# Optimization experiments

Measured on AMD Instinct MI355X. Metric: run time of the kernel, lower is better.

Reference implementation:

```python
import jax, jax.numpy as jnp
import numpy as np

VOCAB = 50000
B, S = 256, 512
M1, M2, EMB = 1024, 512, 256


def setup_inputs() -> dict:
    key = jax.random.key(0)
    k_idx, k1, k2, k3, kb1, kb2, kb3 = jax.random.split(key, 7)
    idx = jax.random.randint(k_idx, (B, S), 0, VOCAB)
    # torch Linear weights are [out, in]
    W1 = jax.random.normal(k1, (M1, VOCAB), dtype=jnp.float32) * (1.0 / np.sqrt(VOCAB))
    b1 = jax.random.normal(kb1, (M1,), dtype=jnp.float32) * 0.01
    W2 = jax.random.normal(k2, (M2, M1), dtype=jnp.float32) * (1.0 / np.sqrt(M1))
    b2 = jax.random.normal(kb2, (M2,), dtype=jnp.float32) * 0.01
    W3 = jax.random.normal(k3, (EMB, M2), dtype=jnp.float32) * (1.0 / np.sqrt(M2))
    b3 = jax.random.normal(kb3, (EMB,), dtype=jnp.float32) * 0.01
    return {"idx": idx, "W1": W1, "b1": b1, "W2": W2, "b2": b2, "W3": W3, "b3": b3}


def make_bow_vector(idx, vocab_size):
    # vectorized scatter-add histogram: vec[i, idx[i, j]] += 1
    batch = idx.shape[0]
    rows = jnp.arange(batch)[:, None]  # [B, 1] broadcast against [B, S]
    return jnp.zeros((batch, vocab_size), dtype=jnp.float32).at[rows, idx].add(1.0)


def reference(idx, W1, b1, W2, b2, W3, b3):
    bow = make_bow_vector(idx, W1.shape[1])            # [B, V]
    h = jax.nn.relu(bow @ W1.T + b1)                   # [B, M1]
    h = jax.nn.relu(h @ W2.T + b2)                     # [B, M2]
    emb = jax.nn.relu(h @ W3.T + b3)                   # [B, EMB]
    return emb
```

## Files before the change

### kernel.cpp

```cpp
#include <hip/hip_runtime.h>
#include <hip/hip_bf16.h>

#define VOCAB   50000
#define BATCH   256
#define SEQ     512
#define NM1     1024
#define NM2     512
#define NEMB    256
#define KB1     782
#define KPAD    (KB1*64)
#define SPLITK  32
#define NT      16
#define HHALF   (KPAD/2)

typedef __attribute__((ext_vector_type(8))) short short8;
typedef __attribute__((ext_vector_type(4))) float f32x4;

#define BOW_BYTES   ((size_t)BATCH * KPAD * 2)
#define PART_BYTES  ((size_t)SPLITK * BATCH * NM1 * 4)

__device__ __forceinline__ short f2b(float x) {
    __hip_bfloat16 b = __float2bfloat16(x);
    return __builtin_bit_cast(short, b);
}
__device__ __forceinline__ unsigned short f2bu(float x) {
    __hip_bfloat16 b = __float2bfloat16(x);
    return __builtin_bit_cast(unsigned short, b);
}

__global__ __launch_bounds__(256) void BOW_hist2(const int* __restrict__ idx,
                                                 __hip_bfloat16* __restrict__ bow) {
    __shared__ unsigned int h[HHALF / 2];
    const int b    = blockIdx.x;
    const int row  = b >> 1;
    const int lo   = (b & 1) * HHALF;
    const int t    = threadIdx.x;

    for (int j = t; j < HHALF / 2; j += 256) h[j] = 0u;
    __syncthreads();

    #pragma unroll
    for (int u = 0; u < 2; u++) {
        int v = idx[row * SEQ + u * 256 + t];
        int d = v - lo;
        if ((unsigned)d < (unsigned)HHALF)
            atomicAdd(&h[d >> 1], (d & 1) ? 0x10000u : 1u);
    }
    __syncthreads();

    unsigned int* dst = (unsigned int*)(bow + (size_t)row * KPAD + lo);
    for (int j = t; j < HHALF / 2; j += 256) {
        unsigned int w  = h[j];
        unsigned int l16 = f2bu((float)(w & 0xFFFFu));
        unsigned int h16 = f2bu((float)(w >> 16));
        dst[j] = l16 | (h16 << 16);
    }
}

__global__ __launch_bounds__(512) void BOW_gemm1(
        const __hip_bfloat16* __restrict__ bow,
        const float* __restrict__ W1,
        float* __restrict__ partials)
{
    __shared__ __align__(16) __hip_bfloat16 As[256 * 64];
    __shared__ __align__(16) __hip_bfloat16 Bs[64 * 64];

    const int tid = threadIdx.x;
    const int bid = blockIdx.x;
    const int s   = bid >> 4;
    const int nt  = bid & 15;
    const int n0  = nt * 64;

    const int kb_start = s * 24 + (s < 14 ? s : 14);
    const int kb_count = 24 + (s < 14 ? 1 : 0);

    const int lane = tid & 63;
    const int w    = tid >> 6;
    const int wm   = w >> 1;
    const int wn   = w & 1;

    f32x4 acc[4][2];
    #pragma unroll
    for (int m = 0; m < 4; m++)
        #pragma unroll
        for (int n = 0; n < 2; n++) acc[m][n] = (f32x4){0.f, 0.f, 0.f, 0.f};

    const int brow = tid >> 3;
    const int bk8  = tid & 7;
    const int bdst = brow * 64 + ((bk8 * 8) ^ ((brow & 7) << 3));
    const float* wsrc = W1 + (size_t)(n0 + brow) * VOCAB + bk8 * 8;

    for (int kb = kb_start; kb < kb_start + kb_count; ++kb) {
        const int kg0 = kb * 64;

        #pragma unroll
        for (int i = 0; i < 4; i++) {
            int c   = i * 512 + tid;
            int row = c >> 3;
            int k8  = c & 7;
            const __hip_bfloat16* src =
                bow + (size_t)row * KPAD + kg0 + ((k8 * 8) ^ ((row & 7) << 3));
            __builtin_amdgcn_global_load_lds(
                (const __attribute__((address_space(1))) void*)src,
                (__attribute__((address_space(3))) void*)&As[c * 8], 16, 0, 0);
        }

        {
            int kg = kg0 + bk8 * 8;
            float4 v0 = {0.f,0.f,0.f,0.f}, v1 = {0.f,0.f,0.f,0.f};
            if (kg < VOCAB) {
                const float* src = wsrc + kg0;
                v0 = *reinterpret_cast<const float4*>(src);
                v1 = *reinterpret_cast<const float4*>(src + 4);
            }
            short8 p;
            p[0] = f2b(v0.x); p[1] = f2b(v0.y); p[2] = f2b(v0.z); p[3] = f2b(v0.w);
            p[4] = f2b(v1.x); p[5] = f2b(v1.y); p[6] = f2b(v1.z); p[7] = f2b(v1.w);
            *reinterpret_cast<short8*>(&Bs[bdst]) = p;
        }
        __syncthreads();

        #pragma unroll
        for (int kk = 0; kk < 2; kk++) {
            short8 a[4], b[2];
            const int kf = kk * 32 + ((lane >> 4) << 3);
            #pragma unroll
            for (int m = 0; m < 4; m++) {
                int row = wm * 64 + m * 16 + (lane & 15);
                int e   = row * 64 + (kf ^ ((row & 7) << 3));
                a[m] = *reinterpret_cast<const short8*>(&As[e]);
            }
            #pragma unroll
            for (int n = 0; n < 2; n++) {
                int row = wn * 32 + n * 16 + (lane & 15);
                int e   = row * 64 + (kf ^ ((row & 7) << 3));
                b[n] = *reinterpret_cast<const short8*>(&Bs[e]);
            }
            #pragma unroll
            for (int m = 0; m < 4; m++)
                #pragma unroll
                for (int n = 0; n < 2; n++)
                    acc[m][n] = __builtin_amdgcn_mfma_f32_16x16x32_bf16(
                                    a[m], b[n], acc[m][n], 0, 0, 0);
        }
        __syncthreads();
    }

    float* dst = partials + (size_t)s * (BATCH * NM1);
    #pragma unroll
    for (int m = 0; m < 4; m++) {
        #pragma unroll
        for (int n = 0; n < 2; n++) {
            int col = n0 + wn * 32 + n * 16 + (lane & 15);
            #pragma unroll
            for (int j = 0; j < 4; j++) {
                int rowi = wm * 64 + m * 16 + ((lane >> 4) * 4 + j);
                dst[(size_t)rowi * NM1 + col] = acc[m][n][j];
            }
        }
    }
}

__global__ void BOW_reduce1(const float* __restrict__ partials,
                            const float* __restrict__ b1,
                            float* __restrict__ h1) {
    int o = blockIdx.x * 256 + threadIdx.x;
    int m = o & (NM1 - 1);
    float s = b1[m];
    #pragma unroll
    for (int sp = 0; sp < SPLITK; sp++) s += partials[(size_t)sp * (BATCH * NM1) + o];
    h1[o] = fmaxf(s, 0.f);
}

__global__ void BOW_gemm_f32(const float* __restrict__ A,
                             const float* __restrict__ Bw,
                             const float* __restrict__ bias,
                             float* __restrict__ out,
                             int N, int K) {
    __shared__ float As[32][33];
    __shared__ float Bs[32][33];
    int tid = threadIdx.x;
    int i0 = blockIdx.y * 32, n0 = blockIdx.x * 32;
    int r = tid >> 5, c = tid & 31;
    int ty = tid >> 4, tx = tid & 15;
    float a2[2][2] = {{0.f, 0.f}, {0.f, 0.f}};

    for (int k0 = 0; k0 < K; k0 += 32) {
        #pragma unroll
        for (int rr = 0; rr < 4; rr++) {
            As[r + rr * 8][c] = A[(size_t)(i0 + r + rr * 8) * K + k0 + c];
            Bs[r + rr * 8][c] = Bw[(size_t)(n0 + r + rr * 8) * K + k0 + c];
        }
        __syncthreads();
        #pragma unroll
        for (int k = 0; k < 32; k++) {
            float av0 = As[ty * 2][k],     av1 = As[ty * 2 + 1][k];
            float bv0 = Bs[tx * 2][k],     bv1 = Bs[tx * 2 + 1][k];
            a2[0][0] += av0 * bv0; a2[0][1] += av0 * bv1;
            a2[1][0] += av1 * bv0; a2[1][1] += av1 * bv1;
        }
        __syncthreads();
    }
    #pragma unroll
    for (int ii = 0; ii < 2; ii++)
        #pragma unroll
        for (int nn = 0; nn < 2; nn++) {
            int i = i0 + ty * 2 + ii, n = n0 + tx * 2 + nn;
            out[(size_t)i * N + n] = fmaxf(a2[ii][nn] + bias[n], 0.f);
        }
}

extern "C" void kernel_launch(void* const* d_in, const int* in_sizes, int n_in,
                              void* d_out, int out_size, void* d_ws, size_t ws_size,
                              hipStream_t stream) {
    const int*   idx = (const int*)d_in[0];
    const float* W1  = (const float*)d_in[1];
    const float* b1  = (const float*)d_in[2];
    const float* W2  = (const float*)d_in[3];
    const float* b2  = (const float*)d_in[4];
    const float* W3  = (const float*)d_in[5];
    const float* b3  = (const float*)d_in[6];
    float* out = (float*)d_out;

    char* ws = (char*)d_ws;
    __hip_bfloat16* bow = (__hip_bfloat16*)ws;
    float* partials = (float*)(ws + BOW_BYTES);
    float* h1       = (float*)(ws + BOW_BYTES + PART_BYTES);
    float* h2       = h1 + BATCH * NM1;

    BOW_hist2<<<BATCH * 2, 256, 0, stream>>>(idx, bow);
    BOW_gemm1<<<SPLITK * NT, 512, 0, stream>>>(bow, W1, partials);
    BOW_reduce1<<<(BATCH * NM1) / 256, 256, 0, stream>>>(partials, b1, h1);
    BOW_gemm_f32<<<dim3(NM2 / 32, BATCH / 32), 256, 0, stream>>>(h1, W2, b2, h2, NM2, NM1);
    BOW_gemm_f32<<<dim3(NEMB / 32, BATCH / 32), 256, 0, stream>>>(h2, W3, b3, out, NEMB, NM2);
}
```

Baseline: 405.5 us.

## Double-buffer LDS tiles in split-K GEMM1 and swizzle block order

Double-buffers the A (bow) and B (W1) shared-memory tiles in the first GEMM, so global loads for the next k-block are issued before the MFMA compute on the current one and each iteration needs one barrier instead of two. It also remaps the block index so that consecutively scheduled blocks work on different split-K slices. LDS use doubles to about 80 KB per block, which may lower occupancy. Relying on global_load_lds writes into the other buffer while computing assumes the barrier orders those asynchronous loads correctly.

```diff
diff --git a/kernel.cpp b/kernel.cpp
--- a/kernel.cpp
+++ b/kernel.cpp
@@ -50,7 +50,7 @@
 
     unsigned int* dst = (unsigned int*)(bow + (size_t)row * KPAD + lo);
     for (int j = t; j < HHALF / 2; j += 256) {
-        unsigned int w  = h[j];
+        unsigned int w   = h[j];
         unsigned int l16 = f2bu((float)(w & 0xFFFFu));
         unsigned int h16 = f2bu((float)(w >> 16));
         dst[j] = l16 | (h16 << 16);
@@ -62,13 +62,13 @@
         const float* __restrict__ W1,
         float* __restrict__ partials)
 {
-    __shared__ __align__(16) __hip_bfloat16 As[256 * 64];
-    __shared__ __align__(16) __hip_bfloat16 Bs[64 * 64];
+    __shared__ __align__(16) __hip_bfloat16 As[2][256 * 64];
+    __shared__ __align__(16) __hip_bfloat16 Bs[2][64 * 64];
 
     const int tid = threadIdx.x;
-    const int bid = blockIdx.x;
-    const int s   = bid >> 4;
-    const int nt  = bid & 15;
+    const int swz = (blockIdx.x & 7) * 64 + (blockIdx.x >> 3);
+    const int s   = swz >> 4;
+    const int nt  = swz & 15;
     const int n0  = nt * 64;
 
     const int kb_start = s * 24 + (s < 14 ? s : 14);
@@ -88,11 +88,10 @@
     const int brow = tid >> 3;
     const int bk8  = tid & 7;
     const int bdst = brow * 64 + ((bk8 * 8) ^ ((brow & 7) << 3));
-    const float* wsrc = W1 + (size_t)(n0 + brow) * VOCAB + bk8 * 8;
-
-    for (int kb = kb_start; kb < kb_start + kb_count; ++kb) {
+    const float* wbase = W1 + (size_t)(n0 + brow) * VOCAB + bk8 * 8;
+
+    auto STAGE_A = [&](int buf, int kb) {
         const int kg0 = kb * 64;
-
         #pragma unroll
         for (int i = 0; i < 4; i++) {
             int c   = i * 512 + tid;
@@ -102,24 +101,26 @@
                 bow + (size_t)row * KPAD + kg0 + ((k8 * 8) ^ ((row & 7) << 3));
             __builtin_amdgcn_global_load_lds(
                 (const __attribute__((address_space(1))) void*)src,
-                (__attribute__((address_space(3))) void*)&As[c * 8], 16, 0, 0);
-        }
-
-        {
-            int kg = kg0 + bk8 * 8;
-            float4 v0 = {0.f,0.f,0.f,0.f}, v1 = {0.f,0.f,0.f,0.f};
-            if (kg < VOCAB) {
-                const float* src = wsrc + kg0;
-                v0 = *reinterpret_cast<const float4*>(src);
-                v1 = *reinterpret_cast<const float4*>(src + 4);
-            }
-            short8 p;
-            p[0] = f2b(v0.x); p[1] = f2b(v0.y); p[2] = f2b(v0.z); p[3] = f2b(v0.w);
-            p[4] = f2b(v1.x); p[5] = f2b(v1.y); p[6] = f2b(v1.z); p[7] = f2b(v1.w);
-            *reinterpret_cast<short8*>(&Bs[bdst]) = p;
-        }
-        __syncthreads();
-
+                (__attribute__((address_space(3))) void*)&As[buf][c * 8], 16, 0, 0);
+        }
+    };
+    auto B_LOAD = [&](int kb, float4& v0, float4& v1) {
+        int kg = kb * 64 + bk8 * 8;
+        v0 = (float4){0.f, 0.f, 0.f, 0.f};
+        v1 = (float4){0.f, 0.f, 0.f, 0.f};
+        if (kg < VOCAB) {
+            const float* src = wbase + kb * 64;
+            v0 = *reinterpret_cast<const float4*>(src);
+            v1 = *reinterpret_cast<const float4*>(src + 4);
+        }
+    };
+    auto B_WRITE = [&](int buf, float4 v0, float4 v1) {
+        short8 p;
+        p[0] = f2b(v0.x); p[1] = f2b(v0.y); p[2] = f2b(v0.z); p[3] = f2b(v0.w);
+        p[4] = f2b(v1.x); p[5] = f2b(v1.y); p[6] = f2b(v1.z); p[7] = f2b(v1.w);
+        *reinterpret_cast<short8*>(&Bs[buf][bdst]) = p;
+    };
+    auto COMPUTE = [&](int buf) {
         #pragma unroll
         for (int kk = 0; kk < 2; kk++) {
             short8 a[4], b[2];
@@ -128,13 +129,13 @@
             for (int m = 0; m < 4; m++) {
                 int row = wm * 64 + m * 16 + (lane & 15);
                 int e   = row * 64 + (kf ^ ((row & 7) << 3));
-                a[m] = *reinterpret_cast<const short8*>(&As[e]);
+                a[m] = *reinterpret_cast<const short8*>(&As[buf][e]);
             }
             #pragma unroll
             for (int n = 0; n < 2; n++) {
                 int row = wn * 32 + n * 16 + (lane & 15);
                 int e   = row * 64 + (kf ^ ((row & 7) << 3));
-                b[n] = *reinterpret_cast<const short8*>(&Bs[e]);
+                b[n] = *reinterpret_cast<const short8*>(&Bs[buf][e]);
             }
             #pragma unroll
             for (int m = 0; m < 4; m++)
@@ -143,8 +144,28 @@
                     acc[m][n] = __builtin_amdgcn_mfma_f32_16x16x32_bf16(
                                     a[m], b[n], acc[m][n], 0, 0, 0);
         }
+    };
+
+    STAGE_A(0, kb_start);
+    {
+        float4 v0, v1;
+        B_LOAD(kb_start, v0, v1);
+        B_WRITE(0, v0, v1);
+    }
+    __syncthreads();
+
+    int cur = 0;
+    for (int kb = kb_start; kb < kb_start + kb_count - 1; ++kb) {
+        int nxt = cur ^ 1;
+        STAGE_A(nxt, kb + 1);
+        float4 v0, v1;
+        B_LOAD(kb + 1, v0, v1);
+        COMPUTE(cur);
+        B_WRITE(nxt, v0, v1);
         __syncthreads();
-    }
+        cur = nxt;
+    }
+    COMPUTE(cur);
 
     float* dst = partials + (size_t)s * (BATCH * NM1);
     #pragma unroll
```

Result: no change. 406.4 us (+0.2%).
